# Kernel tuning notes

Measured on AMD Instinct MI355X. Metric: run time of the kernel, lower is better.

Reference implementation:

```python
import jax, jax.numpy as jnp
import numpy as np

NUM_HEADS = 16


def setup_inputs() -> dict:
    k0 = jax.random.key(0)
    ks = jax.random.split(k0, 5)
    T, S, N, E = 1024, 1024, 8, 1024
    query = jax.random.normal(ks[0], (T, N, E), dtype=jnp.float32)
    key_t = jax.random.normal(ks[1], (S, N, E), dtype=jnp.float32)
    value = jax.random.normal(ks[2], (S, N, E), dtype=jnp.float32)
    # xavier-uniform-like scale for in_proj (fan_in=fan_out-ish): gain*sqrt(6/(3E+E))
    lim_in = float(np.sqrt(6.0 / (3 * E + E)))
    in_proj_weight = jax.random.uniform(ks[3], (3 * E, E), dtype=jnp.float32, minval=-lim_in, maxval=lim_in)
    in_proj_bias = jnp.zeros((3 * E,), dtype=jnp.float32)
    lim_out = float(np.sqrt(1.0 / E))
    out_proj_weight = jax.random.uniform(ks[4], (E, E), dtype=jnp.float32, minval=-lim_out, maxval=lim_out)
    out_proj_bias = jnp.zeros((E,), dtype=jnp.float32)
    return {
        'query': query, 'key': key_t, 'value': value,
        'in_proj_weight': in_proj_weight, 'in_proj_bias': in_proj_bias,
        'out_proj_weight': out_proj_weight, 'out_proj_bias': out_proj_bias,
    }


def reference(query, key, value, in_proj_weight, in_proj_bias, out_proj_weight, out_proj_bias):
    # Faithful to the source: q,k,v ALL come from `query` via the 3E in-projection
    # (the torch code projects only `query` and chunks; key/value tensors unused).
    T, N, E = query.shape
    S = key.shape[0]  # must equal T for the reshape, as in the torch code
    H = NUM_HEADS
    D = E // H
    qkv = jnp.einsum('tne,fe->tnf', query, in_proj_weight) + in_proj_bias  # (T,N,3E)
    q, k, v = jnp.split(qkv, 3, axis=-1)
    q = q * (float(D) ** -0.5)
    # (T, N*H, D) -> (N*H, T, D)
    q = q.reshape(T, N * H, D).transpose(1, 0, 2)
    k = k.reshape(S, N * H, D).transpose(1, 0, 2)
    v = v.reshape(S, N * H, D).transpose(1, 0, 2)
    attn = jnp.einsum('btd,bsd->bts', q, k)          # (N*H, T, S)
    attn = jax.nn.softmax(attn, axis=-1)
    out = jnp.einsum('bts,bsd->btd', attn, v)        # (N*H, T, D)
    out = out.transpose(1, 0, 2).reshape(T, N, E)
    out = jnp.einsum('tne,fe->tnf', out, out_proj_weight) + out_proj_bias
    avg_weights = attn.reshape(N, H, T, S).mean(axis=1)  # (N, T, S)
    return out, avg_weights
```

## Files before the change

kernel.cpp:

```cpp
#include <hip/hip_runtime.h>


typedef __bf16 bf16x8 __attribute__((ext_vector_type(8)));
typedef float f32x4 __attribute__((ext_vector_type(4)));
typedef unsigned int u32;
typedef const __attribute__((address_space(1))) u32 gu32;
typedef __attribute__((address_space(3))) u32 lu32;

#define MFMA(a, b, c) __builtin_amdgcn_mfma_f32_16x16x32_bf16((a), (b), (c), 0, 0, 0)

#if __has_builtin(__builtin_amdgcn_exp2f)
#define EXP2(x) __builtin_amdgcn_exp2f(x)
#else
#define EXP2(x) exp2f(x)
#endif

__device__ __forceinline__ unsigned short f2bf(float x) {
    union { float f; unsigned u; } v; v.f = x;
    unsigned r = v.u + 0x7fffu + ((v.u >> 16) & 1u);
    return (unsigned short)(r >> 16);
}

__device__ __forceinline__ bf16x8 frag_ld(const unsigned short* p) {
    return __builtin_bit_cast(bf16x8, *(const uint4*)p);
}

template<int ROWS>
__device__ __forceinline__ void stageNx64(const unsigned short* g, int gs,
                                          unsigned short* lds, int wave, int lane) {
#pragma unroll
    for (int it = 0; it < ROWS / 32; it++) {
        int chunk = wave * (ROWS / 32) + it;
        int row = chunk * 8 + (lane >> 3);
        int cb = (lane & 7) ^ (row & 7);
        const unsigned short* gp = g + (size_t)row * gs + cb * 8;
        unsigned short* lp = lds + chunk * 512;
        __builtin_amdgcn_global_load_lds((gu32*)gp, (lu32*)lp, 16, 0, 0);
    }
}

__device__ __forceinline__ void stage_half8(const unsigned short* g,
                                            unsigned short* lds, int wave, int lane) {
#pragma unroll
    for (int it = 0; it < 2; it++) {
        int chunk = wave * 2 + it;
        int row = chunk * 8 + (lane >> 3);
        int cb = (lane & 7) ^ (row & 7);
        const unsigned short* gp = g + (size_t)row * 1024 + cb * 8;
        unsigned short* lp = lds + chunk * 512;
        __builtin_amdgcn_global_load_lds((gu32*)gp, (lu32*)lp, 16, 0, 0);
    }
}

__device__ __forceinline__ bf16x8 frag_sw(const unsigned short* lds, int row, int cb) {
    return frag_ld(lds + row * 64 + ((cb ^ (row & 7)) << 3));
}

__global__ void k_convert_all(const float* __restrict__ q, const float* __restrict__ wi,
                              const float* __restrict__ wo,
                              unsigned short* __restrict__ xq, unsigned short* __restrict__ xwi,
                              unsigned short* __restrict__ xwo) {
    int i = blockIdx.x * 256 + threadIdx.x;
    const float* src; unsigned short* dst; int off;
    if (i < 2097152)      { src = q;  dst = xq;  off = i; }
    else if (i < 2883584) { src = wi; dst = xwi; off = i - 2097152; }
    else                  { src = wo; dst = xwo; off = i - 2883584; }
    float4 v = ((const float4*)src)[off];
    ushort4 o;
    o.x = f2bf(v.x); o.y = f2bf(v.y); o.z = f2bf(v.z); o.w = f2bf(v.w);
    ((ushort4*)dst)[off] = o;
}

__global__ __launch_bounds__(512, 2) void k_inproj8(
    const unsigned short* __restrict__ A, const unsigned short* __restrict__ B,
    const float* __restrict__ bias,
    unsigned short* __restrict__ qbf, unsigned short* __restrict__ kbf,
    unsigned short* __restrict__ vTbf)
{
    extern __shared__ unsigned short smem[];
    unsigned short* As = smem;
    unsigned short* Bs = smem + 32768;
    const int tid = threadIdx.x;
    const int wave = tid >> 6, lane = tid & 63;
    const int quad = lane >> 4, l16 = lane & 15;
    const int wm = wave >> 2, wn = wave & 3;
    const int m0 = blockIdx.x * 256, n0 = blockIdx.y * 256;
    const unsigned short* Ab = A + (size_t)m0 * 1024;
    const unsigned short* Bb = B + (size_t)n0 * 1024;

    f32x4 acc[8][4];
#pragma unroll
    for (int i = 0; i < 8; i++)
#pragma unroll
        for (int j = 0; j < 4; j++) acc[i][j] = (f32x4){0.f, 0.f, 0.f, 0.f};

    stage_half8(Bb,                  Bs,                 wave, lane);
    stage_half8(Bb + 128 * 1024,     Bs + 8192,          wave, lane);
    stage_half8(Ab,                  As,                 wave, lane);
    stage_half8(Ab + 128 * 1024,     As + 8192,          wave, lane);
    stage_half8(Bb + 64,             Bs + 16384,         wave, lane);
    stage_half8(Bb + 128 * 1024 + 64, Bs + 16384 + 8192, wave, lane);
    asm volatile("s_waitcnt vmcnt(4)" ::: "memory");
    __builtin_amdgcn_s_barrier();

    bf16x8 a[4][2], b0[2][2], b1[2][2];
#pragma unroll 2
    for (int t = 0; t < 16; t++) {
        unsigned short* Ac = As + (t & 1) * 16384;
        unsigned short* Bc = Bs + (t & 1) * 16384;
        const unsigned short* An = Ab + (size_t)(t + 1) * 64;
        unsigned short* Asn = As + ((t + 1) & 1) * 16384;
        const unsigned short* Bn = Bb + (size_t)(t + 2) * 64;
        unsigned short* Bsn = Bs + (t & 1) * 16384;

#pragma unroll
        for (int i = 0; i < 4; i++)
#pragma unroll
            for (int kc = 0; kc < 2; kc++)
                a[i][kc] = frag_sw(Ac, wm * 128 + i * 16 + l16, kc * 4 + quad);
#pragma unroll
        for (int j = 0; j < 2; j++)
#pragma unroll
            for (int kc = 0; kc < 2; kc++)
                b0[j][kc] = frag_sw(Bc, wn * 64 + j * 16 + l16, kc * 4 + quad);
        if (t < 15) stage_half8(An, Asn, wave, lane);
        asm volatile("s_waitcnt lgkmcnt(8)" ::: "memory");
        __builtin_amdgcn_s_barrier();
        asm volatile("s_waitcnt lgkmcnt(0)" ::: "memory");
        __builtin_amdgcn_s_setprio(1);
#pragma unroll
        for (int i = 0; i < 4; i++)
#pragma unroll
            for (int j = 0; j < 2; j++)
#pragma unroll
                for (int kc = 0; kc < 2; kc++)
                    acc[i][j] = MFMA(a[i][kc], b0[j][kc], acc[i][j]);
        __builtin_amdgcn_s_setprio(0);
        __builtin_amdgcn_s_barrier();

#pragma unroll
        for (int j = 0; j < 2; j++)
#pragma unroll
            for (int kc = 0; kc < 2; kc++)
                b1[j][kc] = frag_sw(Bc, wn * 64 + (j + 2) * 16 + l16, kc * 4 + quad);
        if (t < 15) stage_half8(An + 128 * 1024, Asn + 8192, wave, lane);
        __builtin_amdgcn_s_barrier();
        asm volatile("s_waitcnt lgkmcnt(0)" ::: "memory");
        __builtin_amdgcn_s_setprio(1);
#pragma unroll
        for (int i = 0; i < 4; i++)
#pragma unroll
            for (int j = 0; j < 2; j++)
#pragma unroll
                for (int kc = 0; kc < 2; kc++)
                    acc[i][j + 2] = MFMA(a[i][kc], b1[j][kc], acc[i][j + 2]);
        __builtin_amdgcn_s_setprio(0);
        __builtin_amdgcn_s_barrier();

#pragma unroll
        for (int i = 0; i < 4; i++)
#pragma unroll
            for (int kc = 0; kc < 2; kc++)
                a[i][kc] = frag_sw(Ac, wm * 128 + (i + 4) * 16 + l16, kc * 4 + quad);
        if (t < 14) stage_half8(Bn, Bsn, wave, lane);
        __builtin_amdgcn_s_barrier();
        asm volatile("s_waitcnt lgkmcnt(0)" ::: "memory");
        __builtin_amdgcn_s_setprio(1);
#pragma unroll
        for (int i = 0; i < 4; i++)
#pragma unroll
            for (int j = 0; j < 2; j++)
#pragma unroll
                for (int kc = 0; kc < 2; kc++)
                    acc[i + 4][j + 2] = MFMA(a[i][kc], b1[j][kc], acc[i + 4][j + 2]);
        __builtin_amdgcn_s_setprio(0);
        __builtin_amdgcn_s_barrier();

        if (t < 14) stage_half8(Bn + 128 * 1024, Bsn + 8192, wave, lane);
        __builtin_amdgcn_s_barrier();
        asm volatile("s_waitcnt lgkmcnt(0)" ::: "memory");
        __builtin_amdgcn_s_setprio(1);
#pragma unroll
        for (int i = 0; i < 4; i++)
#pragma unroll
            for (int j = 0; j < 2; j++)
#pragma unroll
                for (int kc = 0; kc < 2; kc++)
                    acc[i + 4][j] = MFMA(a[i][kc], b0[j][kc], acc[i + 4][j]);
        __builtin_amdgcn_s_setprio(0);
        if (t < 14) {
            asm volatile("s_waitcnt vmcnt(4)" ::: "memory");
        } else if (t == 14) {
            asm volatile("s_waitcnt vmcnt(0)" ::: "memory");
        }
        __builtin_amdgcn_s_barrier();
    }

    const float QSCALE = 0.125f * 1.4426950408889634f;
    const int c = n0 >> 10;
#pragma unroll
    for (int i = 0; i < 8; i++) {
#pragma unroll
        for (int j = 0; j < 4; j++) {
            int col = n0 + wn * 64 + j * 16 + l16;
            float bv = bias[col];
            int hd = col & 1023, h = hd >> 6, d = hd & 63;
#pragma unroll
            for (int r = 0; r < 4; r++) {
                int row = m0 + wm * 128 + i * 16 + quad * 4 + r;
                int t = row >> 3, n = row & 7;
                int b = n * 16 + h;
                float val = acc[i][j][r] + bv;
                if (c == 0)      qbf[(size_t)b * 65536 + t * 64 + d] = f2bf(val * QSCALE);
                else if (c == 1) kbf[(size_t)b * 65536 + t * 64 + d] = f2bf(val);
                else             vTbf[(size_t)b * 65536 + (size_t)d * 1024 + t] = f2bf(val);
            }
        }
    }
}

__global__ __launch_bounds__(256) void k_pv(
    const unsigned short* __restrict__ qbf, const unsigned short* __restrict__ kbf,
    const unsigned short* __restrict__ vTbf,
    float* __restrict__ il_g, unsigned short* __restrict__ Obf)
{
    __shared__ unsigned short Ks[2][64 * 64];
    __shared__ unsigned short Vs[2][64 * 64];
    __shared__ unsigned short Ps[128 * 64];
    const int tid = threadIdx.x;
    const int wave = tid >> 6, lane = tid & 63, quad = lane >> 4, l16 = lane & 15;
    const int blk = blockIdx.x;
    const int xcd = blk & 7, idx = blk >> 3;
    const int b = xcd * 16 + (idx >> 3);
    const int t0 = (idx & 7) * 128;
    const int n = b >> 4, h = b & 15;
    const size_t bb = (size_t)b * 65536;

    bf16x8 aq[2][2];
#pragma unroll
    for (int rf = 0; rf < 2; rf++)
#pragma unroll
        for (int kh = 0; kh < 2; kh++)
            aq[rf][kh] = frag_ld(&qbf[bb + (size_t)(t0 + wave * 32 + rf * 16 + l16) * 64 + kh * 32 + quad * 8]);

    float lsum[2][4];
    f32x4 o[2][4];
#pragma unroll
    for (int rf = 0; rf < 2; rf++)
#pragma unroll
        for (int r = 0; r < 4; r++) lsum[rf][r] = 0.f;
#pragma unroll
    for (int rf = 0; rf < 2; rf++)
#pragma unroll
        for (int df = 0; df < 4; df++) o[rf][df] = (f32x4){0.f, 0.f, 0.f, 0.f};

    stageNx64<64>(kbf + bb, 64, Ks[0], wave, lane);
    stageNx64<64>(vTbf + bb, 1024, Vs[0], wave, lane);
    __syncthreads();
    for (int st = 0; st < 16; st++) {
        const int cur = st & 1;
        if (st < 15) {
            stageNx64<64>(kbf + bb + (size_t)((st + 1) * 64) * 64, 64, Ks[cur ^ 1], wave, lane);
            stageNx64<64>(vTbf + bb + (st + 1) * 64, 1024, Vs[cur ^ 1], wave, lane);
        }
#pragma unroll
        for (int cf = 0; cf < 4; cf++) {
            bf16x8 k0 = frag_sw(Ks[cur], cf * 16 + l16, quad);
            bf16x8 k1 = frag_sw(Ks[cur], cf * 16 + l16, 4 + quad);
#pragma unroll
            for (int rf = 0; rf < 2; rf++) {
                f32x4 z = (f32x4){0.f, 0.f, 0.f, 0.f};
                z = MFMA(aq[rf][0], k0, z);
                z = MFMA(aq[rf][1], k1, z);
#pragma unroll
                for (int r = 0; r < 4; r++) {
                    float p = EXP2(z[r]);
                    lsum[rf][r] += p;
                    int prow = wave * 32 + rf * 16 + quad * 4 + r;
                    int col = cf * 16 + l16;
                    Ps[prow * 64 + (((col >> 3) ^ (prow & 7)) << 3) + (col & 7)] = f2bf(p);
                }
            }
        }
#pragma unroll
        for (int kc = 0; kc < 2; kc++) {
            bf16x8 ap0 = frag_sw(Ps, wave * 32 + l16, kc * 4 + quad);
            bf16x8 ap1 = frag_sw(Ps, wave * 32 + 16 + l16, kc * 4 + quad);
#pragma unroll
            for (int df = 0; df < 4; df++) {
                bf16x8 bv = frag_sw(Vs[cur], df * 16 + l16, kc * 4 + quad);
                o[0][df] = MFMA(ap0, bv, o[0][df]);
                o[1][df] = MFMA(ap1, bv, o[1][df]);
            }
        }
        __syncthreads();
    }
#pragma unroll
    for (int rf = 0; rf < 2; rf++)
#pragma unroll
        for (int r = 0; r < 4; r++) {
            float s = lsum[rf][r];
            s += __shfl_xor(s, 1); s += __shfl_xor(s, 2);
            s += __shfl_xor(s, 4); s += __shfl_xor(s, 8);
            lsum[rf][r] = 1.0f / s;
        }
#pragma unroll
    for (int rf = 0; rf < 2; rf++)
#pragma unroll
        for (int df = 0; df < 4; df++)
#pragma unroll
            for (int r = 0; r < 4; r++) {
                int t = t0 + wave * 32 + rf * 16 + quad * 4 + r;
                Obf[(size_t)(t * 8 + n) * 1024 + h * 64 + df * 16 + l16] = f2bf(o[rf][df][r] * lsum[rf][r]);
            }
    if (l16 == 0) {
#pragma unroll
        for (int rf = 0; rf < 2; rf++)
#pragma unroll
            for (int r = 0; r < 4; r++)
                il_g[(size_t)b * 1024 + t0 + wave * 32 + rf * 16 + quad * 4 + r] = lsum[rf][r];
    }
}

__global__ __launch_bounds__(256) void k_avg(
    const unsigned short* __restrict__ qbf, const unsigned short* __restrict__ kbf,
    const float* __restrict__ il_g, float* __restrict__ avg)
{
    __shared__ unsigned short Qs[2][128 * 64];
    __shared__ unsigned short Ks[2][128 * 64];
    __shared__ float Is[16 * 128];
    const int tid = threadIdx.x;
    const int wave = tid >> 6, lane = tid & 63, quad = lane >> 4, l16 = lane & 15;
    const int wm = wave >> 1, wn = wave & 1;
    const int blk = blockIdx.x;
    const int n = blk & 7, idx = blk >> 3;
    const int s0 = (idx & 7) * 128, t0 = (idx >> 3) * 128;

    for (int i2 = tid; i2 < 2048; i2 += 256)
        Is[i2] = il_g[(size_t)(n * 16 + (i2 >> 7)) * 1024 + t0 + (i2 & 127)];

    f32x4 acc[4][4];
#pragma unroll
    for (int i = 0; i < 4; i++)
#pragma unroll
        for (int j = 0; j < 4; j++) acc[i][j] = (f32x4){0.f, 0.f, 0.f, 0.f};

    stageNx64<128>(qbf + (size_t)(n * 16) * 65536 + (size_t)t0 * 64, 64, Qs[0], wave, lane);
    stageNx64<128>(kbf + (size_t)(n * 16) * 65536 + (size_t)s0 * 64, 64, Ks[0], wave, lane);
    __syncthreads();
    for (int h = 0; h < 16; h++) {
        const int cur = h & 1;
        if (h < 15) {
            const size_t bb1 = (size_t)(n * 16 + h + 1) * 65536;
            stageNx64<128>(qbf + bb1 + (size_t)t0 * 64, 64, Qs[cur ^ 1], wave, lane);
            stageNx64<128>(kbf + bb1 + (size_t)s0 * 64, 64, Ks[cur ^ 1], wave, lane);
        }
        bf16x8 af[4][2];
        float ir[4][4];
#pragma unroll
        for (int i = 0; i < 4; i++) {
            af[i][0] = frag_sw(Qs[cur], wm * 64 + i * 16 + l16, quad);
            af[i][1] = frag_sw(Qs[cur], wm * 64 + i * 16 + l16, 4 + quad);
#pragma unroll
            for (int r = 0; r < 4; r++) ir[i][r] = Is[h * 128 + wm * 64 + i * 16 + quad * 4 + r];
        }
#pragma unroll
        for (int j = 0; j < 4; j++) {
            bf16x8 b0 = frag_sw(Ks[cur], wn * 64 + j * 16 + l16, quad);
            bf16x8 b1 = frag_sw(Ks[cur], wn * 64 + j * 16 + l16, 4 + quad);
#pragma unroll
            for (int i = 0; i < 4; i++) {
                f32x4 z = (f32x4){0.f, 0.f, 0.f, 0.f};
                z = MFMA(af[i][0], b0, z);
                z = MFMA(af[i][1], b1, z);
#pragma unroll
                for (int r = 0; r < 4; r++)
                    acc[i][j][r] += EXP2(z[r]) * ir[i][r];
            }
        }
        __syncthreads();
    }
#pragma unroll
    for (int i = 0; i < 4; i++)
#pragma unroll
        for (int j = 0; j < 4; j++)
#pragma unroll
            for (int r = 0; r < 4; r++) {
                int t = t0 + wm * 64 + i * 16 + quad * 4 + r;
                int s = s0 + wn * 64 + j * 16 + l16;
                avg[(size_t)n * 1048576 + (size_t)t * 1024 + s] = acc[i][j][r] * 0.0625f;
            }
}

__global__ __launch_bounds__(256) void k_outproj(
    const unsigned short* __restrict__ A, const unsigned short* __restrict__ B,
    const float* __restrict__ bias, float* __restrict__ out)
{
    __shared__ unsigned short As[2][128 * 64];
    __shared__ unsigned short Bs[2][128 * 64];
    const int tid = threadIdx.x;
    const int wave = tid >> 6, lane = tid & 63;
    const int quad = lane >> 4, l16 = lane & 15;
    const int wm = wave >> 1, wn = wave & 1;
    const int m0 = blockIdx.x * 128, n0 = blockIdx.y * 128;
    const unsigned short* Ab = A + (size_t)m0 * 1024;
    const unsigned short* Bb = B + (size_t)n0 * 1024;

    f32x4 acc[4][4];
#pragma unroll
    for (int i = 0; i < 4; i++)
#pragma unroll
        for (int j = 0; j < 4; j++) acc[i][j] = (f32x4){0.f, 0.f, 0.f, 0.f};

    stageNx64<128>(Ab, 1024, As[0], wave, lane);
    stageNx64<128>(Bb, 1024, Bs[0], wave, lane);
    __syncthreads();
    for (int it = 0; it < 16; it++) {
        const int cur = it & 1;
        if (it < 15) {
            stageNx64<128>(Ab + (it + 1) * 64, 1024, As[cur ^ 1], wave, lane);
            stageNx64<128>(Bb + (it + 1) * 64, 1024, Bs[cur ^ 1], wave, lane);
        }
#pragma unroll
        for (int kc = 0; kc < 2; kc++) {
            bf16x8 af[4], bfr[4];
#pragma unroll
            for (int i = 0; i < 4; i++) af[i]  = frag_sw(As[cur], wm * 64 + i * 16 + l16, kc * 4 + quad);
#pragma unroll
            for (int j = 0; j < 4; j++) bfr[j] = frag_sw(Bs[cur], wn * 64 + j * 16 + l16, kc * 4 + quad);
#pragma unroll
            for (int i = 0; i < 4; i++)
#pragma unroll
                for (int j = 0; j < 4; j++) acc[i][j] = MFMA(af[i], bfr[j], acc[i][j]);
        }
        __syncthreads();
    }
#pragma unroll
    for (int i = 0; i < 4; i++)
#pragma unroll
        for (int j = 0; j < 4; j++) {
            int col = n0 + wn * 64 + j * 16 + l16;
            float bv = bias[col];
#pragma unroll
            for (int r = 0; r < 4; r++) {
                int row = m0 + wm * 64 + i * 16 + quad * 4 + r;
                out[(size_t)row * 1024 + col] = acc[i][j][r] + bv;
            }
        }
}

extern "C" void kernel_launch(void* const* d_in, const int* in_sizes, int n_in,
                              void* d_out, int out_size, void* d_ws, size_t ws_size,
                              hipStream_t stream)
{
    const float* query = (const float*)d_in[0];
    const float* w_in  = (const float*)d_in[3];
    const float* b_in  = (const float*)d_in[4];
    const float* w_out = (const float*)d_in[5];
    const float* b_out = (const float*)d_in[6];
    float* out = (float*)d_out;
    float* avg = out + 8388608;

    if (ws_size < ((size_t)73 << 20)) return;

    static bool attr_set = false;
    if (!attr_set) {
        (void)hipFuncSetAttribute((const void*)k_inproj8,
                                  hipFuncAttributeMaxDynamicSharedMemorySize, 131072);
        attr_set = true;
    }

    char* ws = (char*)d_ws;
    unsigned short* qbf  = (unsigned short*)(ws);
    unsigned short* kbf  = (unsigned short*)(ws + ((size_t)16 << 20));
    unsigned short* vTbf = (unsigned short*)(ws + ((size_t)32 << 20));
    unsigned short* xbf  = (unsigned short*)(ws + ((size_t)48 << 20));
    unsigned short* wibf = (unsigned short*)(ws + ((size_t)64 << 20));
    unsigned short* wobf = (unsigned short*)(ws + ((size_t)70 << 20));
    float* il_g = (float*)(ws + ((size_t)72 << 20));

    k_convert_all<<<12288, 256, 0, stream>>>(query, w_in, w_out, xbf, wibf, wobf);
    k_inproj8<<<dim3(32, 12), 512, 131072, stream>>>(xbf, wibf, b_in, qbf, kbf, vTbf);
    k_pv    <<<1024, 256, 0, stream>>>(qbf, kbf, vTbf, il_g, xbf);
    k_avg   <<<512, 256, 0, stream>>>(qbf, kbf, il_g, avg);
    k_outproj<<<dim3(64, 8), 256, 0, stream>>>(xbf, wobf, b_out, out);
}
```

Measured before the change: 374.1 us.

## Retile in-projection to 256x128, store Q/K row-major, and swizzle block order

```diff
diff --git a/kernel.cpp b/kernel.cpp
--- a/kernel.cpp
+++ b/kernel.cpp
@@ -83,53 +83,52 @@
     const int tid = threadIdx.x;
     const int wave = tid >> 6, lane = tid & 63;
     const int quad = lane >> 4, l16 = lane & 15;
-    const int wm = wave >> 2, wn = wave & 3;
-    const int m0 = blockIdx.x * 256, n0 = blockIdx.y * 256;
+    const int wm = wave >> 1, wn = wave & 1;
+    const int bx = blockIdx.x;
+    const int mx = (bx & 7) * 4 + (bx >> 3);
+    const int m0 = mx * 256, n0 = blockIdx.y * 128;
     const unsigned short* Ab = A + (size_t)m0 * 1024;
     const unsigned short* Bb = B + (size_t)n0 * 1024;
 
-    f32x4 acc[8][4];
-#pragma unroll
-    for (int i = 0; i < 8; i++)
+    f32x4 acc[4][4];
+#pragma unroll
+    for (int i = 0; i < 4; i++)
 #pragma unroll
         for (int j = 0; j < 4; j++) acc[i][j] = (f32x4){0.f, 0.f, 0.f, 0.f};
 
-    stage_half8(Bb,                  Bs,                 wave, lane);
-    stage_half8(Bb + 128 * 1024,     Bs + 8192,          wave, lane);
-    stage_half8(Ab,                  As,                 wave, lane);
-    stage_half8(Ab + 128 * 1024,     As + 8192,          wave, lane);
-    stage_half8(Bb + 64,             Bs + 16384,         wave, lane);
-    stage_half8(Bb + 128 * 1024 + 64, Bs + 16384 + 8192, wave, lane);
-    asm volatile("s_waitcnt vmcnt(4)" ::: "memory");
+    stage_half8(Ab,              As,        wave, lane);
+    stage_half8(Ab + 128 * 1024, As + 8192, wave, lane);
+    stage_half8(Bb,              Bs,        wave, lane);
+    stage_half8(Bb + 64,         Bs + 8192, wave, lane);
+    asm volatile("s_waitcnt vmcnt(2)" ::: "memory");
     __builtin_amdgcn_s_barrier();
 
-    bf16x8 a[4][2], b0[2][2], b1[2][2];
+    bf16x8 a[2][2], b0[2][2], b1[2][2];
 #pragma unroll 2
     for (int t = 0; t < 16; t++) {
         unsigned short* Ac = As + (t & 1) * 16384;
-        unsigned short* Bc = Bs + (t & 1) * 16384;
+        unsigned short* Bc = Bs + (t & 1) * 8192;
+        unsigned short* Asn = As + ((t + 1) & 1) * 16384;
+        unsigned short* Bsn = Bs + (t & 1) * 8192;
         const unsigned short* An = Ab + (size_t)(t + 1) * 64;
-        unsigned short* Asn = As + ((t + 1) & 1) * 16384;
         const unsigned short* Bn = Bb + (size_t)(t + 2) * 64;
-        unsigned short* Bsn = Bs + (t & 1) * 16384;
-
-#pragma unroll
-        for (int i = 0; i < 4; i++)
+
+#pragma unroll
+        for (int i = 0; i < 2; i++)
 #pragma unroll
             for (int kc = 0; kc < 2; kc++)
-                a[i][kc] = frag_sw(Ac, wm * 128 + i * 16 + l16, kc * 4 + quad);
+                a[i][kc] = frag_sw(Ac, wm * 64 + i * 16 + l16, kc * 4 + quad);
 #pragma unroll
         for (int j = 0; j < 2; j++)
 #pragma unroll
             for (int kc = 0; kc < 2; kc++)
                 b0[j][kc] = frag_sw(Bc, wn * 64 + j * 16 + l16, kc * 4 + quad);
         if (t < 15) stage_half8(An, Asn, wave, lane);
-        asm volatile("s_waitcnt lgkmcnt(8)" ::: "memory");
         __builtin_amdgcn_s_barrier();
         asm volatile("s_waitcnt lgkmcnt(0)" ::: "memory");
         __builtin_amdgcn_s_setprio(1);
 #pragma unroll
-        for (int i = 0; i < 4; i++)
+        for (int i = 0; i < 2; i++)
 #pragma unroll
             for (int j = 0; j < 2; j++)
 #pragma unroll
@@ -148,7 +147,7 @@
         asm volatile("s_waitcnt lgkmcnt(0)" ::: "memory");
         __builtin_amdgcn_s_setprio(1);
 #pragma unroll
-        for (int i = 0; i < 4; i++)
+        for (int i = 0; i < 2; i++)
 #pragma unroll
             for (int j = 0; j < 2; j++)
 #pragma unroll
@@ -158,38 +157,35 @@
         __builtin_amdgcn_s_barrier();
 
 #pragma unroll
-        for (int i = 0; i < 4; i++)
+        for (int i = 0; i < 2; i++)
 #pragma unroll
             for (int kc = 0; kc < 2; kc++)
-                a[i][kc] = frag_sw(Ac, wm * 128 + (i + 4) * 16 + l16, kc * 4 + quad);
+                a[i][kc] = frag_sw(Ac, wm * 64 + (i + 2) * 16 + l16, kc * 4 + quad);
         if (t < 14) stage_half8(Bn, Bsn, wave, lane);
         __builtin_amdgcn_s_barrier();
         asm volatile("s_waitcnt lgkmcnt(0)" ::: "memory");
         __builtin_amdgcn_s_setprio(1);
 #pragma unroll
-        for (int i = 0; i < 4; i++)
+        for (int i = 0; i < 2; i++)
 #pragma unroll
             for (int j = 0; j < 2; j++)
 #pragma unroll
                 for (int kc = 0; kc < 2; kc++)
-                    acc[i + 4][j + 2] = MFMA(a[i][kc], b1[j][kc], acc[i + 4][j + 2]);
+                    acc[i + 2][j + 2] = MFMA(a[i][kc], b1[j][kc], acc[i + 2][j + 2]);
         __builtin_amdgcn_s_setprio(0);
         __builtin_amdgcn_s_barrier();
 
-        if (t < 14) stage_half8(Bn + 128 * 1024, Bsn + 8192, wave, lane);
-        __builtin_amdgcn_s_barrier();
-        asm volatile("s_waitcnt lgkmcnt(0)" ::: "memory");
         __builtin_amdgcn_s_setprio(1);
 #pragma unroll
-        for (int i = 0; i < 4; i++)
+        for (int i = 0; i < 2; i++)
 #pragma unroll
             for (int j = 0; j < 2; j++)
 #pragma unroll
                 for (int kc = 0; kc < 2; kc++)
-                    acc[i + 4][j] = MFMA(a[i][kc], b0[j][kc], acc[i + 4][j]);
+                    acc[i + 2][j] = MFMA(a[i][kc], b0[j][kc], acc[i + 2][j]);
         __builtin_amdgcn_s_setprio(0);
         if (t < 14) {
-            asm volatile("s_waitcnt vmcnt(4)" ::: "memory");
+            asm volatile("s_waitcnt vmcnt(2)" ::: "memory");
         } else if (t == 14) {
             asm volatile("s_waitcnt vmcnt(0)" ::: "memory");
         }
@@ -199,21 +195,24 @@
     const float QSCALE = 0.125f * 1.4426950408889634f;
     const int c = n0 >> 10;
 #pragma unroll
-    for (int i = 0; i < 8; i++) {
+    for (int i = 0; i < 4; i++) {
 #pragma unroll
         for (int j = 0; j < 4; j++) {
             int col = n0 + wn * 64 + j * 16 + l16;
             float bv = bias[col];
-            int hd = col & 1023, h = hd >> 6, d = hd & 63;
+            int hd = col & 1023;
 #pragma unroll
             for (int r = 0; r < 4; r++) {
-                int row = m0 + wm * 128 + i * 16 + quad * 4 + r;
-                int t = row >> 3, n = row & 7;
-                int b = n * 16 + h;
+                int row = m0 + wm * 64 + i * 16 + quad * 4 + r;
                 float val = acc[i][j][r] + bv;
-                if (c == 0)      qbf[(size_t)b * 65536 + t * 64 + d] = f2bf(val * QSCALE);
-                else if (c == 1) kbf[(size_t)b * 65536 + t * 64 + d] = f2bf(val);
-                else             vTbf[(size_t)b * 65536 + (size_t)d * 1024 + t] = f2bf(val);
+                if (c == 0)      qbf[(size_t)row * 1024 + hd] = f2bf(val * QSCALE);
+                else if (c == 1) kbf[(size_t)row * 1024 + hd] = f2bf(val);
+                else {
+                    int h = hd >> 6, d = hd & 63;
+                    int t = row >> 3, n = row & 7;
+                    int b = n * 16 + h;
+                    vTbf[(size_t)b * 65536 + (size_t)d * 1024 + t] = f2bf(val);
+                }
             }
         }
     }
@@ -234,14 +233,15 @@
     const int b = xcd * 16 + (idx >> 3);
     const int t0 = (idx & 7) * 128;
     const int n = b >> 4, h = b & 15;
-    const size_t bb = (size_t)b * 65536;
+    const size_t vb = (size_t)b * 65536;
+    const size_t qkb = (size_t)n * 1024 + h * 64;
 
     bf16x8 aq[2][2];
 #pragma unroll
     for (int rf = 0; rf < 2; rf++)
 #pragma unroll
         for (int kh = 0; kh < 2; kh++)
-            aq[rf][kh] = frag_ld(&qbf[bb + (size_t)(t0 + wave * 32 + rf * 16 + l16) * 64 + kh * 32 + quad * 8]);
+            aq[rf][kh] = frag_ld(&qbf[(size_t)(t0 + wave * 32 + rf * 16 + l16) * 8192 + qkb + kh * 32 + quad * 8]);
 
     float lsum[2][4];
     f32x4 o[2][4];
@@ -254,14 +254,14 @@
 #pragma unroll
         for (int df = 0; df < 4; df++) o[rf][df] = (f32x4){0.f, 0.f, 0.f, 0.f};
 
-    stageNx64<64>(kbf + bb, 64, Ks[0], wave, lane);
-    stageNx64<64>(vTbf + bb, 1024, Vs[0], wave, lane);
+    stageNx64<64>(kbf + qkb, 8192, Ks[0], wave, lane);
+    stageNx64<64>(vTbf + vb, 1024, Vs[0], wave, lane);
     __syncthreads();
     for (int st = 0; st < 16; st++) {
         const int cur = st & 1;
         if (st < 15) {
-            stageNx64<64>(kbf + bb + (size_t)((st + 1) * 64) * 64, 64, Ks[cur ^ 1], wave, lane);
-            stageNx64<64>(vTbf + bb + (st + 1) * 64, 1024, Vs[cur ^ 1], wave, lane);
+            stageNx64<64>(kbf + qkb + (size_t)(st + 1) * 524288, 8192, Ks[cur ^ 1], wave, lane);
+            stageNx64<64>(vTbf + vb + (st + 1) * 64, 1024, Vs[cur ^ 1], wave, lane);
         }
 #pragma unroll
         for (int cf = 0; cf < 4; cf++) {
@@ -345,15 +345,16 @@
 #pragma unroll
         for (int j = 0; j < 4; j++) acc[i][j] = (f32x4){0.f, 0.f, 0.f, 0.f};
 
-    stageNx64<128>(qbf + (size_t)(n * 16) * 65536 + (size_t)t0 * 64, 64, Qs[0], wave, lane);
-    stageNx64<128>(kbf + (size_t)(n * 16) * 65536 + (size_t)s0 * 64, 64, Ks[0], wave, lane);
+    const size_t qb = (size_t)t0 * 8192 + (size_t)n * 1024;
+    const size_t kb = (size_t)s0 * 8192 + (size_t)n * 1024;
+    stageNx64<128>(qbf + qb, 8192, Qs[0], wave, lane);
+    stageNx64<128>(kbf + kb, 8192, Ks[0], wave, lane);
     __syncthreads();
     for (int h = 0; h < 16; h++) {
         const int cur = h & 1;
         if (h < 15) {
-            const size_t bb1 = (size_t)(n * 16 + h + 1) * 65536;
-            stageNx64<128>(qbf + bb1 + (size_t)t0 * 64, 64, Qs[cur ^ 1], wave, lane);
-            stageNx64<128>(kbf + bb1 + (size_t)s0 * 64, 64, Ks[cur ^ 1], wave, lane);
+            stageNx64<128>(qbf + qb + (h + 1) * 64, 8192, Qs[cur ^ 1], wave, lane);
+            stageNx64<128>(kbf + kb + (h + 1) * 64, 8192, Ks[cur ^ 1], wave, lane);
         }
         bf16x8 af[4][2];
         float ir[4][4];
@@ -402,7 +403,9 @@
     const int wave = tid >> 6, lane = tid & 63;
     const int quad = lane >> 4, l16 = lane & 15;
     const int wm = wave >> 1, wn = wave & 1;
-    const int m0 = blockIdx.x * 128, n0 = blockIdx.y * 128;
+    const int bx = blockIdx.x;
+    const int mx = (bx & 7) * 8 + (bx >> 3);
+    const int m0 = mx * 128, n0 = blockIdx.y * 128;
     const unsigned short* Ab = A + (size_t)m0 * 1024;
     const unsigned short* Bb = B + (size_t)n0 * 1024;
 
@@ -466,7 +469,7 @@
     static bool attr_set = false;
     if (!attr_set) {
         (void)hipFuncSetAttribute((const void*)k_inproj8,
-                                  hipFuncAttributeMaxDynamicSharedMemorySize, 131072);
+                                  hipFuncAttributeMaxDynamicSharedMemorySize, 98304);
         attr_set = true;
     }
 
@@ -480,7 +483,7 @@
     float* il_g = (float*)(ws + ((size_t)72 << 20));
 
     k_convert_all<<<12288, 256, 0, stream>>>(query, w_in, w_out, xbf, wibf, wobf);
-    k_inproj8<<<dim3(32, 12), 512, 131072, stream>>>(xbf, wibf, b_in, qbf, kbf, vTbf);
+    k_inproj8<<<dim3(32, 24), 512, 98304, stream>>>(xbf, wibf, b_in, qbf, kbf, vTbf);
     k_pv    <<<1024, 256, 0, stream>>>(qbf, kbf, vTbf, il_g, xbf);
     k_avg   <<<512, 256, 0, stream>>>(qbf, kbf, il_g, avg);
     k_outproj<<<dim3(64, 8), 256, 0, stream>>>(xbf, wobf, b_out, out);
```

Measured after the change: 342.1 us. 8.5% less time.
